# Performance work log

Measured on AMD Instinct MI355X. Metric: run time of the kernel, lower is better.

The kernel has to match this reference:

```python
import jax, jax.numpy as jnp
import numpy as np

DIAG_W = 0.707  # diagonal neighbor weight from original code
# 3x3 Gaussian weights (1/16)*[[1,2,1],[2,4,2],[1,2,1]]
GAUSS = np.array([[1., 2., 1.], [2., 4., 2.], [1., 2., 4.]], dtype=np.float32)
GAUSS = np.array([[1., 2., 1.], [2., 4., 2.], [1., 2., 1.]], dtype=np.float32) / 16.0


def sml(x):
    # x: [B,C,H,W]; 8-neighbor abs-diff stencil with clamped (edge-replicate) borders
    p = jnp.pad(x, ((0, 0), (0, 0), (1, 1), (1, 1)), mode='edge')
    c = p[..., 1:-1, 1:-1]
    up, dn = p[..., :-2, 1:-1], p[..., 2:, 1:-1]
    lf, rt = p[..., 1:-1, :-2], p[..., 1:-1, 2:]
    ul, ur = p[..., :-2, :-2], p[..., :-2, 2:]
    dl, dr = p[..., 2:, :-2], p[..., 2:, 2:]
    ortho = jnp.abs(c - up) + jnp.abs(c - dn) + jnp.abs(c - lf) + jnp.abs(c - rt)
    diag = jnp.abs(c - ul) + jnp.abs(c - dr) + jnp.abs(c - ur) + jnp.abs(c - dl)
    return ortho + DIAG_W * diag


def nsml(x):
    # x: [B,C,H,W] already rescaled; zero-pad SML, then Gaussian-weighted sum of SQUARES
    s = sml(x)
    sq = jnp.pad(s, ((0, 0), (0, 0), (1, 1), (1, 1)), mode='constant') ** 2
    H, W = s.shape[-2], s.shape[-1]
    out = jnp.zeros_like(s)
    for di in range(3):
        for dj in range(3):
            out = out + GAUSS[di, dj] * sq[..., di:di + H, dj:dj + W]
    return out


def get_nsml_tensor(t):
    return nsml((t + 1.0) / 2.0)


def setup_inputs() -> dict:
    key = jax.random.key(0)
    ka, kb = jax.random.split(key)
    shape = (16, 3, 1024, 1024)
    return {
        'TensorA': jax.random.normal(ka, shape, dtype=jnp.float32),
        'TensorB': jax.random.normal(kb, shape, dtype=jnp.float32),
    }


def reference(TensorA, TensorB):
    LA = get_nsml_tensor(TensorA)
    LB = get_nsml_tensor(TensorB)
    return jnp.mean((LA - LB) ** 2)
```

## Files before the change

### kernel.cpp

```cpp
#include <hip/hip_runtime.h>

#define NT     256
#define TILE   64
#define XROWS  70
#define XCOLS  72
#define XLOADC 70
#define DDW    68
#define PH     1024
#define PW     1024
#define NMT    289

__device__ __forceinline__ int iclamp(int v, int hi) {
    return v < 0 ? 0 : (v > hi ? hi : v);
}

extern "C" __global__ void __launch_bounds__(NT, 4)
nsml_loss_kernel(const float* __restrict__ A, const float* __restrict__ B,
                 double* __restrict__ acc) {
    __shared__ float xs[XROWS][XCOLS];
    __shared__ float dd[DDW][DDW];
    __shared__ float wpart[NT / 64];

    const int tid = threadIdx.x;
    const int ox  = blockIdx.x * TILE;
    const int oy  = blockIdx.y * TILE;
    const size_t base = (size_t)blockIdx.z * (size_t)(PH * PW);

    const bool vecok = (ox >= 2) && (ox + 68 <= PW);

    for (int pass = 0; pass < 2; ++pass) {
        const float* __restrict__ src = (pass == 0 ? A : B) + base;

        if (vecok) {
            for (int idx = tid; idx < XROWS * 35; idx += NT) {
                int r  = idx / 35, c2 = idx - r * 35;
                int gy = iclamp(oy - 2 + r, PH - 1);
                const float2 v = *(const float2*)&src[(size_t)gy * PW + (ox - 2) + c2 * 2];
                float2 w;
                w.x = 0.5f * (v.x + 1.0f);
                w.y = 0.5f * (v.y + 1.0f);
                *(float2*)&xs[r][c2 * 2] = w;
            }
        } else {
            for (int idx = tid; idx < XROWS * XLOADC; idx += NT) {
                int r  = idx / XLOADC, c = idx - r * XLOADC;
                int gy = iclamp(oy - 2 + r, PH - 1);
                int gx = iclamp(ox - 2 + c, PW - 1);
                xs[r][c] = 0.5f * (src[(size_t)gy * PW + gx] + 1.0f);
            }
        }
        __syncthreads();

        for (int m = tid; m < NMT; m += NT) {
            int q0 = (m % 17) * 4;
            int p0 = (m / 17) * 4;
            float r[6][8];
            #pragma unroll
            for (int i = 0; i < 6; ++i) {
                float4 a = *(const float4*)&xs[p0 + i][q0];
                float4 b = *(const float4*)&xs[p0 + i][q0 + 4];
                r[i][0] = a.x; r[i][1] = a.y; r[i][2] = a.z; r[i][3] = a.w;
                r[i][4] = b.x; r[i][5] = b.y; r[i][6] = b.z; r[i][7] = b.w;
            }
            #pragma unroll
            for (int i = 0; i < 4; ++i) {
                float o[4];
                #pragma unroll
                for (int j = 0; j < 4; ++j) {
                    float c = r[i + 1][j + 1];
                    float ortho = fabsf(c - r[i][j + 1]) + fabsf(c - r[i + 2][j + 1])
                                + fabsf(c - r[i + 1][j]) + fabsf(c - r[i + 1][j + 2]);
                    float diag  = fabsf(c - r[i][j])     + fabsf(c - r[i + 2][j + 2])
                                + fabsf(c - r[i][j + 2]) + fabsf(c - r[i + 2][j]);
                    float s = ortho + 0.707f * diag;
                    int gy = oy - 1 + p0 + i;
                    int gx = ox - 1 + q0 + j;
                    bool in = ((unsigned)gy < (unsigned)PH) & ((unsigned)gx < (unsigned)PW);
                    o[j] = in ? s * s : 0.0f;
                }
                float4 w = make_float4(o[0], o[1], o[2], o[3]);
                float4* dst = (float4*)&dd[p0 + i][q0];
                if (pass == 0) {
                    *dst = w;
                } else {
                    float4 old = *dst;
                    *dst = make_float4(old.x - w.x, old.y - w.y, old.z - w.z, old.w - w.w);
                }
            }
        }
        __syncthreads();
    }

    float ta = 0.0f;
    {
        int tx0 = (tid & 15) * 4;
        int ty0 = (tid >> 4) * 4;
        float r[6][8];
        #pragma unroll
        for (int i = 0; i < 6; ++i) {
            float4 a = *(const float4*)&dd[ty0 + i][tx0];
            float4 b = *(const float4*)&dd[ty0 + i][tx0 + 4];
            r[i][0] = a.x; r[i][1] = a.y; r[i][2] = a.z; r[i][3] = a.w;
            r[i][4] = b.x; r[i][5] = b.y; r[i][6] = b.z; r[i][7] = b.w;
        }
        float h[6][4];
        #pragma unroll
        for (int i = 0; i < 6; ++i)
            #pragma unroll
            for (int j = 0; j < 4; ++j)
                h[i][j] = r[i][j] + 2.0f * r[i][j + 1] + r[i][j + 2];
        #pragma unroll
        for (int i = 0; i < 4; ++i)
            #pragma unroll
            for (int j = 0; j < 4; ++j) {
                float g = 0.0625f * (h[i][j] + 2.0f * h[i + 1][j] + h[i + 2][j]);
                ta += g * g;
            }
    }

    #pragma unroll
    for (int off = 32; off > 0; off >>= 1) ta += __shfl_down(ta, off, 64);
    if ((tid & 63) == 0) wpart[tid >> 6] = ta;
    __syncthreads();
    if (tid == 0) {
        double t = (double)wpart[0] + (double)wpart[1] + (double)wpart[2] + (double)wpart[3];
        atomicAdd(acc, t);
    }
}

extern "C" __global__ void finalize_kernel(const double* __restrict__ acc,
                                           float* __restrict__ out, double inv_n) {
    out[0] = (float)(acc[0] * inv_n);
}

extern "C" void kernel_launch(void* const* d_in, const int* in_sizes, int n_in,
                              void* d_out, int out_size, void* d_ws, size_t ws_size,
                              hipStream_t stream) {
    const float* A = (const float*)d_in[0];
    const float* B = (const float*)d_in[1];
    float* out  = (float*)d_out;
    double* acc = (double*)d_ws;

    const long long n = (long long)in_sizes[0];
    const int planes  = (int)(n / ((long long)PH * PW));

    hipMemsetAsync(d_ws, 0, sizeof(double), stream);

    dim3 grid(PW / TILE, PH / TILE, planes);
    nsml_loss_kernel<<<grid, NT, 0, stream>>>(A, B, acc);
    finalize_kernel<<<1, 1, 0, stream>>>(acc, out, 1.0 / (double)n);
}
```

Baseline: 532.3 us.

## Replace shared-memory tiled stencil with register-streaming per-thread column strips

The block-tiled kernel that staged halos in LDS is replaced by one where each thread owns an 8-wide column strip over a 32-row band. It streams rows directly from global memory into rolling register buffers, processing A and B together and fusing the SML, square-difference and separable Gaussian in registers. This removes LDS staging, the two-pass structure and the barriers, but adds per-thread halo reloads, wider uncoalesced vector loads and more register pressure.

```diff
diff --git a/kernel.cpp b/kernel.cpp
--- a/kernel.cpp
+++ b/kernel.cpp
@@ -1,130 +1,138 @@
 #include <hip/hip_runtime.h>
 
-#define NT     256
-#define TILE   64
-#define XROWS  70
-#define XCOLS  72
-#define XLOADC 70
-#define DDW    68
-#define PH     1024
-#define PW     1024
-#define NMT    289
+#define PW   1024
+#define PH   1024
+#define SW   8
+#define ROWS 32
+#define NSX  (PW / SW)
+#define NBY  (PH / ROWS)
+#define NT   256
 
-__device__ __forceinline__ int iclamp(int v, int hi) {
-    return v < 0 ? 0 : (v > hi ? hi : v);
-}
+#define AF(v) (((v) + 1.0f) * 0.5f)
 
-extern "C" __global__ void __launch_bounds__(NT, 4)
-nsml_loss_kernel(const float* __restrict__ A, const float* __restrict__ B,
-                 double* __restrict__ acc) {
-    __shared__ float xs[XROWS][XCOLS];
-    __shared__ float dd[DDW][DDW];
+#define P1_0 2
+#define P2_0 1
+#define P1_1 0
+#define P2_1 2
+#define P1_2 1
+#define P2_2 0
+
+#define SVAL(X, p2, p1, kk, c, outv)                                      \
+  {                                                                       \
+    float cen_  = X[p1][(c) + 1];                                         \
+    float orth_ = fabsf(cen_ - X[p2][(c) + 1])                            \
+                + fabsf(cen_ - X[kk][(c) + 1])                            \
+                + fabsf(cen_ - X[p1][(c)])                                \
+                + fabsf(cen_ - X[p1][(c) + 2]);                           \
+    float diag_ = fabsf(cen_ - X[p2][(c)])                                \
+                + fabsf(cen_ - X[kk][(c) + 2])                            \
+                + fabsf(cen_ - X[p2][(c) + 2])                            \
+                + fabsf(cen_ - X[kk][(c)]);                               \
+    outv = fmaf(0.707f, diag_, orth_);                                    \
+  }
+
+#define STORE12(X, k, a2, b4, c4, d2)                                     \
+  X[k][0] = AF(a2.x);  X[k][1] = AF(a2.y);                                \
+  X[k][2] = AF(b4.x);  X[k][3] = AF(b4.y);                                \
+  X[k][4] = AF(b4.z);  X[k][5] = AF(b4.w);                                \
+  X[k][6] = AF(c4.x);  X[k][7] = AF(c4.y);                                \
+  X[k][8] = AF(c4.z);  X[k][9] = AF(c4.w);                                \
+  X[k][10] = AF(d2.x); X[k][11] = AF(d2.y);
+
+#define STEP(k, p2c, p1c)                                                 \
+  {                                                                       \
+    const int rr = t < 0 ? 0 : (t >= PH ? PH - 1 : t);                    \
+    const float* rpA = pA + (size_t)rr * PW;                              \
+    const float* rpB = pB + (size_t)rr * PW;                              \
+    float2 a2A = *(const float2*)(rpA + cm2);                             \
+    float4 b4A = *(const float4*)(rpA + j0);                              \
+    float4 c4A = *(const float4*)(rpA + j0 + 4);                          \
+    float2 d2A = *(const float2*)(rpA + cp2);                             \
+    float2 a2B = *(const float2*)(rpB + cm2);                             \
+    float4 b4B = *(const float4*)(rpB + j0);                              \
+    float4 c4B = *(const float4*)(rpB + j0 + 4);                          \
+    float2 d2B = *(const float2*)(rpB + cp2);                             \
+    if (eL) { a2A.x = b4A.x; a2A.y = b4A.x; a2B.x = b4B.x; a2B.y = b4B.x; } \
+    if (eR) { d2A.x = c4A.w; d2A.y = c4A.w; d2B.x = c4B.w; d2B.y = c4B.w; } \
+    STORE12(xA, k, a2A, b4A, c4A, d2A)                                    \
+    STORE12(xB, k, a2B, b4B, c4B, d2B)                                    \
+    const int sr = t - 1;                                                 \
+    if (sr >= srlo && sr <= srhi) {                                       \
+      float dd[10];                                                       \
+      _Pragma("unroll")                                                   \
+      for (int c = 0; c < 10; ++c) {                                      \
+        float sA_, sB_;                                                   \
+        SVAL(xA, p2c, p1c, k, c, sA_)                                     \
+        SVAL(xB, p2c, p1c, k, c, sB_)                                     \
+        dd[c] = fmaf(sA_, sA_, -(sB_ * sB_));                             \
+      }                                                                   \
+      dd[0] *= mL;                                                        \
+      dd[9] *= mR;                                                        \
+      _Pragma("unroll")                                                   \
+      for (int j = 0; j < 8; ++j)                                         \
+        h[k][j] = fmaf(2.0f, dd[j + 1], dd[j] + dd[j + 2]);               \
+    } else {                                                              \
+      _Pragma("unroll")                                                   \
+      for (int j = 0; j < 8; ++j) h[k][j] = 0.0f;                         \
+    }                                                                     \
+    const int orow = t - 2;                                               \
+    if (orow >= y0 && orow <= yhi) {                                      \
+      _Pragma("unroll")                                                   \
+      for (int j = 0; j < 8; ++j) {                                       \
+        float g = fmaf(2.0f, h[p1c][j], h[p2c][j] + h[k][j]) * 0.0625f;   \
+        facc = fmaf(g, g, facc);                                          \
+      }                                                                   \
+    }                                                                     \
+    ++t;                                                                  \
+  }
+
+extern "C" __global__ void __launch_bounds__(NT, 3)
+nsml_stream_kernel(const float* __restrict__ A, const float* __restrict__ B,
+                   double* __restrict__ acc) {
     __shared__ float wpart[NT / 64];
 
     const int tid = threadIdx.x;
-    const int ox  = blockIdx.x * TILE;
-    const int oy  = blockIdx.y * TILE;
-    const size_t base = (size_t)blockIdx.z * (size_t)(PH * PW);
+    const int gid = blockIdx.x * NT + tid;
+    const int sx   = gid % NSX;
+    const int band = (gid / NSX) % NBY;
+    const int pl   = gid / (NSX * NBY);
 
-    const bool vecok = (ox >= 2) && (ox + 68 <= PW);
+    const int j0 = sx * SW;
+    const int y0 = band * ROWS;
+    const int yhi = y0 + ROWS - 1;
+    const int srlo = (y0 - 1 < 0) ? 0 : (y0 - 1);
+    const int srhi = (y0 + ROWS > PH - 1) ? (PH - 1) : (y0 + ROWS);
 
-    for (int pass = 0; pass < 2; ++pass) {
-        const float* __restrict__ src = (pass == 0 ? A : B) + base;
+    const size_t pbase = (size_t)pl * (size_t)(PH * PW);
+    const float* __restrict__ pA = A + pbase;
+    const float* __restrict__ pB = B + pbase;
 
-        if (vecok) {
-            for (int idx = tid; idx < XROWS * 35; idx += NT) {
-                int r  = idx / 35, c2 = idx - r * 35;
-                int gy = iclamp(oy - 2 + r, PH - 1);
-                const float2 v = *(const float2*)&src[(size_t)gy * PW + (ox - 2) + c2 * 2];
-                float2 w;
-                w.x = 0.5f * (v.x + 1.0f);
-                w.y = 0.5f * (v.y + 1.0f);
-                *(float2*)&xs[r][c2 * 2] = w;
-            }
-        } else {
-            for (int idx = tid; idx < XROWS * XLOADC; idx += NT) {
-                int r  = idx / XLOADC, c = idx - r * XLOADC;
-                int gy = iclamp(oy - 2 + r, PH - 1);
-                int gx = iclamp(ox - 2 + c, PW - 1);
-                xs[r][c] = 0.5f * (src[(size_t)gy * PW + gx] + 1.0f);
-            }
-        }
-        __syncthreads();
+    const bool eL = (sx == 0);
+    const bool eR = (sx == NSX - 1);
+    const float mL = eL ? 0.0f : 1.0f;
+    const float mR = eR ? 0.0f : 1.0f;
+    const int cm2 = eL ? 0 : (j0 - 2);
+    const int cp2 = eR ? (PW - 2) : (j0 + 8);
 
-        for (int m = tid; m < NMT; m += NT) {
-            int q0 = (m % 17) * 4;
-            int p0 = (m / 17) * 4;
-            float r[6][8];
-            #pragma unroll
-            for (int i = 0; i < 6; ++i) {
-                float4 a = *(const float4*)&xs[p0 + i][q0];
-                float4 b = *(const float4*)&xs[p0 + i][q0 + 4];
-                r[i][0] = a.x; r[i][1] = a.y; r[i][2] = a.z; r[i][3] = a.w;
-                r[i][4] = b.x; r[i][5] = b.y; r[i][6] = b.z; r[i][7] = b.w;
-            }
-            #pragma unroll
-            for (int i = 0; i < 4; ++i) {
-                float o[4];
-                #pragma unroll
-                for (int j = 0; j < 4; ++j) {
-                    float c = r[i + 1][j + 1];
-                    float ortho = fabsf(c - r[i][j + 1]) + fabsf(c - r[i + 2][j + 1])
-                                + fabsf(c - r[i + 1][j]) + fabsf(c - r[i + 1][j + 2]);
-                    float diag  = fabsf(c - r[i][j])     + fabsf(c - r[i + 2][j + 2])
-                                + fabsf(c - r[i][j + 2]) + fabsf(c - r[i + 2][j]);
-                    float s = ortho + 0.707f * diag;
-                    int gy = oy - 1 + p0 + i;
-                    int gx = ox - 1 + q0 + j;
-                    bool in = ((unsigned)gy < (unsigned)PH) & ((unsigned)gx < (unsigned)PW);
-                    o[j] = in ? s * s : 0.0f;
-                }
-                float4 w = make_float4(o[0], o[1], o[2], o[3]);
-                float4* dst = (float4*)&dd[p0 + i][q0];
-                if (pass == 0) {
-                    *dst = w;
-                } else {
-                    float4 old = *dst;
-                    *dst = make_float4(old.x - w.x, old.y - w.y, old.z - w.z, old.w - w.w);
-                }
-            }
-        }
-        __syncthreads();
-    }
+    float xA[3][12], xB[3][12];
+    float h[3][8];
+    float facc = 0.0f;
 
-    float ta = 0.0f;
-    {
-        int tx0 = (tid & 15) * 4;
-        int ty0 = (tid >> 4) * 4;
-        float r[6][8];
-        #pragma unroll
-        for (int i = 0; i < 6; ++i) {
-            float4 a = *(const float4*)&dd[ty0 + i][tx0];
-            float4 b = *(const float4*)&dd[ty0 + i][tx0 + 4];
-            r[i][0] = a.x; r[i][1] = a.y; r[i][2] = a.z; r[i][3] = a.w;
-            r[i][4] = b.x; r[i][5] = b.y; r[i][6] = b.z; r[i][7] = b.w;
-        }
-        float h[6][4];
-        #pragma unroll
-        for (int i = 0; i < 6; ++i)
-            #pragma unroll
-            for (int j = 0; j < 4; ++j)
-                h[i][j] = r[i][j] + 2.0f * r[i][j + 1] + r[i][j + 2];
-        #pragma unroll
-        for (int i = 0; i < 4; ++i)
-            #pragma unroll
-            for (int j = 0; j < 4; ++j) {
-                float g = 0.0625f * (h[i][j] + 2.0f * h[i + 1][j] + h[i + 2][j]);
-                ta += g * g;
-            }
+    int t = y0 - 2;
+    for (int it = 0; it < 12; ++it) {
+        STEP(0, P2_0, P1_0)
+        STEP(1, P2_1, P1_1)
+        STEP(2, P2_2, P1_2)
     }
 
     #pragma unroll
-    for (int off = 32; off > 0; off >>= 1) ta += __shfl_down(ta, off, 64);
-    if ((tid & 63) == 0) wpart[tid >> 6] = ta;
+    for (int off = 32; off > 0; off >>= 1) facc += __shfl_down(facc, off, 64);
+    if ((tid & 63) == 0) wpart[tid >> 6] = facc;
     __syncthreads();
     if (tid == 0) {
-        double t = (double)wpart[0] + (double)wpart[1] + (double)wpart[2] + (double)wpart[3];
-        atomicAdd(acc, t);
+        double s = (double)wpart[0] + (double)wpart[1]
+                 + (double)wpart[2] + (double)wpart[3];
+        atomicAdd(acc, s);
     }
 }
 
@@ -146,7 +154,7 @@
 
     hipMemsetAsync(d_ws, 0, sizeof(double), stream);
 
-    dim3 grid(PW / TILE, PH / TILE, planes);
-    nsml_loss_kernel<<<grid, NT, 0, stream>>>(A, B, acc);
+    const int total_threads = NSX * NBY * planes;
+    nsml_stream_kernel<<<total_threads / NT, NT, 0, stream>>>(A, B, acc);
     finalize_kernel<<<1, 1, 0, stream>>>(acc, out, 1.0 / (double)n);
 }
```

After: 428.3 us. -19.5%, faster.
